# Performance work log

Measured on AMD Instinct MI355X. Metric: run time of the kernel, lower is better.

Reference implementation:

```python
import jax, jax.numpy as jnp
import numpy as np

B, S, D_IN, D_SRC, D_OUT = 128, 2048, 1024, 1024, 1024
W = 64                      # window_size
WL = 2 * W + 1              # window_length
STD_SQ = (W / 2.0) ** 2
EPS = 1e-14


def setup_inputs() -> dict:
    key = jax.random.key(0)
    ks = jax.random.split(key, 8)
    inp = jax.random.normal(ks[0], (B, D_IN), dtype=jnp.float32)
    source_hids = jax.random.normal(ks[1], (S, B, D_SRC), dtype=jnp.float32)
    # per-sample valid lengths; must satisfy L <= S - WL so the dynamic window stays in-bounds
    lengths = jax.random.randint(ks[2], (B,), 1024, S - WL + 1)
    encoder_padding_mask = jnp.arange(S)[:, None] >= lengths[None, :]  # [S, B], True = pad
    d_half = (D_IN + 1) // 2
    u = lambda k, shape, a: jax.random.uniform(k, shape, jnp.float32, -a, a)
    Wi = u(ks[3], (D_SRC, D_IN), 0.1)             # input_proj (no bias)
    Wo = u(ks[4], (D_OUT, D_IN + D_SRC), 0.1)     # output_proj (no bias)
    b1_bound = 1.0 / np.sqrt(D_IN)
    W1 = u(ks[5], (d_half, D_IN), b1_bound); b1 = u(ks[5], (d_half,), b1_bound)
    b2_bound = 1.0 / np.sqrt(d_half)
    W2 = u(ks[6], (1, d_half), b2_bound); b2 = u(ks[6], (1,), b2_bound)
    return {"input": inp, "source_hids": source_hids,
            "encoder_padding_mask": encoder_padding_mask,
            "Wi": Wi, "Wo": Wo, "W1": W1, "b1": b1, "W2": W2, "b2": b2}


def reference(input, source_hids, encoder_padding_mask, Wi, Wo, W1, b1, W2, b2):
    lengths = jnp.sum(~encoder_padding_mask, axis=0).astype(jnp.float32)  # [B]
    x = input @ Wi.T                                                      # [B, D_SRC]
    # predicted window center p = W + L * sigmoid(fc2(tanh(fc1(x))))
    p_sig = jax.nn.sigmoid(jnp.tanh(x @ W1.T + b1) @ W2.T + b2)[:, 0]     # [B]
    p = W + lengths * p_sig                                               # [B]
    window_start = jnp.round(p - W).astype(jnp.int32)                     # [B]
    positions = window_start[:, None].astype(jnp.float32) + jnp.arange(WL, dtype=jnp.float32)  # [B, WL]
    # per-sample dynamic window gather from [B, S, D]
    src_bt = jnp.transpose(source_hids, (1, 0, 2))
    selection = jax.vmap(
        lambda s, st: jax.lax.dynamic_slice(s, (st, 0), (WL, s.shape[1]))
    )(src_bt, window_start)                                               # [B, WL, D_SRC]
    gaussian = jnp.exp(-(positions - p[:, None]) ** 2 / (2.0 * STD_SQ))   # [B, WL]
    score = jnp.einsum('bd,bwd->bw', x, selection)                        # [B, WL]
    # valid absolute positions are [W, L + W); outside -> epsilon (matches torch loop)
    valid = (positions >= W) & (positions < lengths[:, None] + W)
    score = jnp.where(valid, score, EPS)
    a = jax.nn.softmax(score, axis=1) * gaussian                          # [B, WL]
    c = jnp.einsum('bw,bwd->bd', a, selection)                            # [B, D_SRC]
    out = jnp.tanh(jnp.concatenate((c, input), axis=1) @ Wo.T)            # [B, D_OUT]
    return out, a, window_start, window_start + WL
```

## Files before the change

### kernel.cpp

```cpp
#include <hip/hip_runtime.h>
#include <math.h>

#define BB   128
#define SS   2048
#define DIN  1024
#define DSRC 1024
#define DOUT 1024
#define WW   64
#define WLEN 129
#define HH   512
#define WCH  17
#define GW   136

#define OFF_WSI   0
#define OFF_P     512
#define OFF_LEN   1024
#define OFF_GTAB  4096
#define OFF_XP    73728
#define OFF_X32   4268032
#define OFF_Z1P   4792320
#define OFF_C32   6889472
#define OFF_CPART 7413760
#define OFF_MPART 11608064
#define OFF_LPART 11612160
#define OFF_SPART 11616256
#define OFF_OP    11685888
#define WS_NEED   15880192

#define DO_A    (BB*DOUT)
#define DO_WS   (DO_A + BB*WLEN)
#define DO_WE   (DO_WS + BB)

template<int NTOT, int KRANGE, bool F64OUT>
__device__ __forceinline__ void gemm16(const int gblk, const int t,
    const float* __restrict__ A, const int lda,
    const float* __restrict__ Wt, const int ldw,
    void* __restrict__ outp, float* __restrict__ alds )
{
    constexpr int NJB = NTOT / 16;
    const int jb = gblk % NJB;
    const int ks = gblk / NJB;
    const int lane = t & 63;
    const int wvid = __builtin_amdgcn_readfirstlane(t >> 6);
    const int j0 = jb * 16 + wvid * 2;
    const int k0 = ks * KRANGE;

    double dac[2][2];
    dac[0][0] = 0.0; dac[0][1] = 0.0; dac[1][0] = 0.0; dac[1][1] = 0.0;

    const float* wbase = Wt + (size_t)j0 * ldw;

    for (int kc = 0; kc < KRANGE; kc += 64) {
        const int kg = k0 + kc;
        __syncthreads();
        #pragma unroll
        for (int q = 0; q < 4; ++q) {
            const int f4 = t + 512 * q;
            const int bb = f4 >> 4, c4 = f4 & 15;
            const float4 v = *reinterpret_cast<const float4*>(A + (size_t)bb * lda + kg + c4 * 4);
            alds[(c4*4+0)*130 + bb] = v.x;
            alds[(c4*4+1)*130 + bb] = v.y;
            alds[(c4*4+2)*130 + bb] = v.z;
            alds[(c4*4+3)*130 + bb] = v.w;
        }
        __syncthreads();
        const float* wr = wbase + kg;
        #pragma unroll
        for (int kk16 = 0; kk16 < 64; kk16 += 16) {
            float fa[2][2];
            fa[0][0] = 0.f; fa[0][1] = 0.f; fa[1][0] = 0.f; fa[1][1] = 0.f;
            #pragma unroll
            for (int kk = 0; kk < 16; ++kk) {
                const int k = kk16 + kk;
                const float2 av = *reinterpret_cast<const float2*>(&alds[k*130 + 2*lane]);
                #pragma unroll
                for (int jj = 0; jj < 2; ++jj) {
                    const float wvv = wr[jj*ldw + k];
                    fa[jj][0] = fmaf(wvv, av.x, fa[jj][0]);
                    fa[jj][1] = fmaf(wvv, av.y, fa[jj][1]);
                }
            }
            #pragma unroll
            for (int jj = 0; jj < 2; ++jj) {
                dac[jj][0] += (double)fa[jj][0];
                dac[jj][1] += (double)fa[jj][1];
            }
        }
    }
    #pragma unroll
    for (int i = 0; i < 2; ++i) {
        const int b = 2*lane + i;
        const size_t base = ((size_t)ks * BB + b) * NTOT + j0;
        if constexpr (F64OUT) {
            double* o = (double*)outp;
            o[base + 0] = dac[0][i];
            o[base + 1] = dac[1][i];
        } else {
            float* o = (float*)outp;
            o[base + 0] = (float)dac[0][i];
            o[base + 1] = (float)dac[1][i];
        }
    }
}

__global__ __launch_bounds__(512)
void k_combo(const float* __restrict__ input, const float* __restrict__ Wi,
             const float* __restrict__ Wo, const unsigned char* __restrict__ mask,
             double* __restrict__ xp, float* __restrict__ op4, int* __restrict__ lengths)
{
    __shared__ __align__(16) float alds[64*130];
    const int blk = blockIdx.x, t = threadIdx.x;
    if (blk < 256) {
        gemm16<1024, 256, true>(blk, t, input, DIN, Wi, DIN, xp, alds);
    } else if (blk < 512) {
        gemm16<1024, 256, false>(blk - 256, t, input, DIN, Wo + 1024, DIN + DSRC, op4, alds);
    } else {
        const int b = blk - 512;
        const bool is_u8 = (mask[(size_t)SS*BB - 1] != 0);
        int cnt = 0;
        if (is_u8) {
            #pragma unroll
            for (int q = 0; q < 4; ++q)
                cnt += (mask[(size_t)(t + 512*q)*BB + b] != 0) ? 1 : 0;
        } else {
            const int* m32 = (const int*)mask;
            #pragma unroll
            for (int q = 0; q < 4; ++q)
                cnt += (m32[(size_t)(t + 512*q)*BB + b] != 0) ? 1 : 0;
        }
        int* red = (int*)alds;
        red[t] = cnt;
        __syncthreads();
        for (int st = 256; st >= 1; st >>= 1) {
            if (t < st) red[t] += red[t + st];
            __syncthreads();
        }
        if (t == 0) lengths[b] = SS - red[0];
    }
}

__global__ __launch_bounds__(512)
void k_xred(const double* __restrict__ xp, float* __restrict__ x32)
{
    const int i = blockIdx.x * 512 + threadIdx.x;
    double s = 0.0;
    #pragma unroll
    for (int ks = 0; ks < 4; ++ks) s += xp[(size_t)ks * (BB*DSRC) + i];
    x32[i] = (float)s;
}

__global__ __launch_bounds__(512)
void k_fc1(const float* __restrict__ x32, const float* __restrict__ W1, double* __restrict__ z1p)
{
    __shared__ __align__(16) float alds[64*130];
    gemm16<512, 256, true>(blockIdx.x, threadIdx.x, x32, DSRC, W1, DIN, z1p, alds);
}

__global__ __launch_bounds__(64)
void k_fc2(const double* __restrict__ z1p, const float* __restrict__ b1,
           const float* __restrict__ W2f, const float* __restrict__ b2,
           const int* __restrict__ lengths, int* __restrict__ wsi,
           float* __restrict__ pbuf, float* __restrict__ gtab, float* __restrict__ dout)
{
    const int b = blockIdx.x, lane = threadIdx.x;
    double part = 0.0;
    #pragma unroll
    for (int q = 0; q < 8; ++q) {
        const int h = lane + 64*q;
        double z = 0.0;
        #pragma unroll
        for (int ks = 0; ks < 4; ++ks) z += z1p[((size_t)ks*BB + b)*HH + h];
        z += (double)b1[h];
        part += tanh(z) * (double)W2f[h];
    }
    #pragma unroll
    for (int off = 32; off >= 1; off >>= 1) part += __shfl_xor(part, off);
    const double z2  = part + (double)b2[0];
    const double sig = 1.0 / (1.0 + exp(-z2));
    const double wsf = (double)lengths[b] * sig;
    int W0 = (int)rint(wsf);
    if (W0 < 0) W0 = 0;
    if (W0 > SS - WLEN) W0 = SS - WLEN;
    const float pf = (float)(wsf + 64.0);
    if (lane == 0) {
        wsi[b]  = W0;
        pbuf[b] = pf;
        dout[DO_WS + b] = (float)W0;
        dout[DO_WE + b] = (float)(W0 + WLEN);
    }
    #pragma unroll
    for (int q = 0; q < 3; ++q) {
        const int w = lane + 64*q;
        if (w < GW) {
            float g = 0.f;
            if (w < WLEN) {
                const float d = (float)(W0 + w) - pf;
                g = expf(d*d * (-1.0f/2048.0f));
            }
            gtab[b*GW + w] = g;
        }
    }
}

__global__ __launch_bounds__(256)
void k_score(const float* __restrict__ x32, const float* __restrict__ src,
             const int* __restrict__ wsi, const float* __restrict__ pbuf,
             const int* __restrict__ lengths, const float* __restrict__ gtab,
             float* __restrict__ cpart, float* __restrict__ mpart,
             float* __restrict__ lpart, float* __restrict__ spart)
{
    const int wc = blockIdx.x, b = blockIdx.y;
    const int t = threadIdx.x, lane = t & 63, wv = t >> 6;
    const int   w0 = wsi[b];
    const int   L  = lengths[b];

    const float4 x4 = *reinterpret_cast<const float4*>(x32 + b*DSRC + 4*t);

    float4 sel[WCH];
    #pragma unroll
    for (int i = 0; i < WCH; ++i) {
        const int w = wc*WCH + i;
        if (w < WLEN) {
            const size_t off = ((size_t)(w0 + w) * BB + b) * DSRC + 4*t;
            sel[i] = *reinterpret_cast<const float4*>(src + off);
        } else sel[i] = make_float4(0.f, 0.f, 0.f, 0.f);
    }

    float w_[32];
    #pragma unroll
    for (int i = 0; i < WCH; ++i)
        w_[i] = fmaf(x4.x, sel[i].x, fmaf(x4.y, sel[i].y, fmaf(x4.z, sel[i].z, x4.w * sel[i].w)));
    #pragma unroll
    for (int i = WCH; i < 32; ++i) w_[i] = 0.f;

    #pragma unroll
    for (int k = 0; k < 5; ++k) {
        const int dist = 1 << k;
        const bool hi = (lane >> k) & 1;
        const int n2 = 32 >> (k + 1);
        #pragma unroll
        for (int i = 0; i < n2; ++i) {
            const float keep = hi ? w_[2*i+1] : w_[2*i];
            const float send = hi ? w_[2*i]   : w_[2*i+1];
            w_[i] = keep + __shfl_xor(send, dist);
        }
    }
    const float tot = w_[0] + __shfl_xor(w_[0], 32);

    __shared__ float red[WCH][4];
    __shared__ float s_sh[WCH];
    if (lane < WCH) red[lane][wv] = tot;
    __syncthreads();
    if (t < WCH) {
        const int w = wc*WCH + t;
        float s;
        if (w < WLEN) {
            const float sum = red[t][0] + red[t][1] + red[t][2] + red[t][3];
            const int pos = w0 + w;
            s = (pos >= WW && pos < L + WW) ? sum : 1e-14f;
        } else s = -INFINITY;
        s_sh[t] = s;
    }
    __syncthreads();

    float sv[WCH];
    #pragma unroll
    for (int i = 0; i < WCH; ++i) sv[i] = s_sh[i];
    float m_loc = -INFINITY;
    #pragma unroll
    for (int i = 0; i < WCH; ++i) m_loc = fmaxf(m_loc, sv[i]);
    float l_loc = 0.f;
    float4 c = make_float4(0.f, 0.f, 0.f, 0.f);
    #pragma unroll
    for (int i = 0; i < WCH; ++i) {
        const float e = expf(sv[i] - m_loc);
        l_loc += e;
        const float g = gtab[b*GW + wc*WCH + i];
        const float wt = e * g;
        c.x = fmaf(wt, sel[i].x, c.x);
        c.y = fmaf(wt, sel[i].y, c.y);
        c.z = fmaf(wt, sel[i].z, c.z);
        c.w = fmaf(wt, sel[i].w, c.w);
    }
    *reinterpret_cast<float4*>(cpart + ((size_t)(b*8 + wc))*DSRC + 4*t) = c;
    if (t == 0) { mpart[b*8 + wc] = m_loc; lpart[b*8 + wc] = l_loc; }
    if (t < WCH) spart[(b*8 + wc)*WCH + t] = s_sh[t];
}

__global__ __launch_bounds__(256)
void k_merge(const float* __restrict__ cpart, const float* __restrict__ mpart,
             const float* __restrict__ lpart, const float* __restrict__ spart,
             const float* __restrict__ gtab, float* __restrict__ c32,
             float* __restrict__ dout)
{
    const int b = blockIdx.x, t = threadIdx.x;
    __shared__ float mv[8], lv[8];
    if (t < 8) { mv[t] = mpart[b*8 + t]; lv[t] = lpart[b*8 + t]; }
    __syncthreads();
    float m = -INFINITY;
    #pragma unroll
    for (int i = 0; i < 8; ++i) m = fmaxf(m, mv[i]);
    float l = 0.f;
    float fac[8];
    #pragma unroll
    for (int i = 0; i < 8; ++i) { fac[i] = expf(mv[i] - m); l = fmaf(lv[i], fac[i], l); }
    const float inv = 1.0f / l;

    float4 c = make_float4(0.f, 0.f, 0.f, 0.f);
    #pragma unroll
    for (int i = 0; i < 8; ++i) {
        const float4 cp = *reinterpret_cast<const float4*>(cpart + ((size_t)(b*8 + i))*DSRC + 4*t);
        c.x = fmaf(cp.x, fac[i], c.x);
        c.y = fmaf(cp.y, fac[i], c.y);
        c.z = fmaf(cp.z, fac[i], c.z);
        c.w = fmaf(cp.w, fac[i], c.w);
    }
    c.x *= inv; c.y *= inv; c.z *= inv; c.w *= inv;
    *reinterpret_cast<float4*>(c32 + (size_t)b*DSRC + 4*t) = c;

    if (t < WLEN) {
        const int wc = t / WCH, i = t % WCH;
        const float s = spart[(b*8 + wc)*WCH + i];
        const float g = gtab[b*GW + t];
        dout[DO_A + b*WLEN + t] = expf(s - m) * inv * g;
    }
}

__global__ __launch_bounds__(512)
void k_gemm2c(const float* __restrict__ c32, const float* __restrict__ Wo, float* __restrict__ op)
{
    __shared__ __align__(16) float alds[64*130];
    gemm16<1024, 256, false>(blockIdx.x, threadIdx.x, c32, DSRC, Wo, DIN + DSRC, op, alds);
}

__global__ __launch_bounds__(512)
void k_outred(const float* __restrict__ op, float* __restrict__ dout)
{
    const int i = blockIdx.x * 512 + threadIdx.x;
    float s = 0.f;
    #pragma unroll
    for (int ks = 0; ks < 8; ++ks) s += op[(size_t)ks * (BB*DOUT) + i];
    dout[i] = tanhf(s);
}

extern "C" void kernel_launch(void* const* d_in, const int* in_sizes, int n_in,
                              void* d_out, int out_size, void* d_ws, size_t ws_size,
                              hipStream_t stream)
{
    const float* input = (const float*)d_in[0];
    const float* src   = (const float*)d_in[1];
    const unsigned char* mask = (const unsigned char*)d_in[2];
    const float* Wi = (const float*)d_in[3];
    const float* Wo = (const float*)d_in[4];
    const float* W1 = (const float*)d_in[5];
    const float* b1 = (const float*)d_in[6];
    const float* W2 = (const float*)d_in[7];
    const float* b2 = (const float*)d_in[8];
    float* out = (float*)d_out;

    if (ws_size < (size_t)WS_NEED) return;

    char* ws = (char*)d_ws;
    int*    wsi     = (int*)   (ws + OFF_WSI);
    float*  pbuf    = (float*) (ws + OFF_P);
    int*    lengths = (int*)   (ws + OFF_LEN);
    float*  gtab    = (float*) (ws + OFF_GTAB);
    double* xp      = (double*)(ws + OFF_XP);
    float*  x32     = (float*) (ws + OFF_X32);
    double* z1p     = (double*)(ws + OFF_Z1P);
    float*  c32     = (float*) (ws + OFF_C32);
    float*  cpart   = (float*) (ws + OFF_CPART);
    float*  mpart   = (float*) (ws + OFF_MPART);
    float*  lpart   = (float*) (ws + OFF_LPART);
    float*  spart   = (float*) (ws + OFF_SPART);
    float*  op      = (float*) (ws + OFF_OP);

    k_combo<<<640, 512, 0, stream>>>(input, Wi, Wo, mask, xp, op + 4*(size_t)BB*DOUT, lengths);
    k_xred<<<256, 512, 0, stream>>>(xp, x32);
    k_fc1<<<128, 512, 0, stream>>>(x32, W1, z1p);
    k_fc2<<<128, 64, 0, stream>>>(z1p, b1, W2, b2, lengths, wsi, pbuf, gtab, out);
    k_score<<<dim3(8,128), 256, 0, stream>>>(x32, src, wsi, pbuf, lengths, gtab,
                                             cpart, mpart, lpart, spart);
    k_merge<<<128, 256, 0, stream>>>(cpart, mpart, lpart, spart, gtab, c32, out);
    k_gemm2c<<<256, 512, 0, stream>>>(c32, Wo, op);
    k_outred<<<256, 512, 0, stream>>>(op, out);
}
```

Measured before the change: 75.55 us.

## Compute Wi and Wo-input GEMMs with full-K per block, drop x reduction kernel

Replaces the split-K gemm16 calls in the first kernel with a custom full-K loop: each wave computes one output column for all 128 batch rows, staging input tiles through LDS with register prefetch. The direct results remove the k_xred launch and its partial-sum buffers, and the output reduction now reads 4 partials plus one direct term. Grid shrinks from 640 to 384 blocks, so there is less parallelism and each block does a longer serial K loop. The x32 buffer is also reused for c32, which is safe only because nothing reads x32 after k_score runs.

```diff
diff --git a/kernel.cpp b/kernel.cpp
--- a/kernel.cpp
+++ b/kernel.cpp
@@ -16,16 +16,15 @@
 #define OFF_P     512
 #define OFF_LEN   1024
 #define OFF_GTAB  4096
-#define OFF_XP    73728
-#define OFF_X32   4268032
-#define OFF_Z1P   4792320
-#define OFF_C32   6889472
-#define OFF_CPART 7413760
-#define OFF_MPART 11608064
-#define OFF_LPART 11612160
-#define OFF_SPART 11616256
-#define OFF_OP    11685888
-#define WS_NEED   15880192
+#define OFF_X32   73728
+#define OFF_OPI   598016
+#define OFF_Z1P   1122304
+#define OFF_CPART 3219456
+#define OFF_MPART 7413760
+#define OFF_LPART 7417856
+#define OFF_SPART 7421952
+#define OFF_OP    7491584
+#define WS_NEED   9588736
 
 #define DO_A    (BB*DOUT)
 #define DO_WS   (DO_A + BB*WLEN)
@@ -106,16 +105,68 @@
 __global__ __launch_bounds__(512)
 void k_combo(const float* __restrict__ input, const float* __restrict__ Wi,
              const float* __restrict__ Wo, const unsigned char* __restrict__ mask,
-             double* __restrict__ xp, float* __restrict__ op4, int* __restrict__ lengths)
+             float* __restrict__ x32, float* __restrict__ opi, int* __restrict__ lengths)
 {
     __shared__ __align__(16) float alds[64*130];
     const int blk = blockIdx.x, t = threadIdx.x;
+    const int lane = t & 63;
+    const int wv = __builtin_amdgcn_readfirstlane(t >> 6);
+
     if (blk < 256) {
-        gemm16<1024, 256, true>(blk, t, input, DIN, Wi, DIN, xp, alds);
-    } else if (blk < 512) {
-        gemm16<1024, 256, false>(blk - 256, t, input, DIN, Wo + 1024, DIN + DSRC, op4, alds);
+        const bool isX = (blk < 128);
+        const int j = (isX ? blk : blk - 128) * 8 + wv;
+        const float* wr0 = isX ? (Wi + (size_t)j * DIN)
+                               : (Wo + (size_t)j * (DIN + DSRC) + 1024);
+        double dac0 = 0.0, dac1 = 0.0;
+
+        float4 pf[4];
+        #pragma unroll
+        for (int q = 0; q < 4; ++q) {
+            const int f4 = t + 512*q;
+            const int bb = f4 >> 4, c4 = f4 & 15;
+            pf[q] = *reinterpret_cast<const float4*>(input + (size_t)bb*DIN + c4*4);
+        }
+        for (int c = 0; c < 16; ++c) {
+            __syncthreads();
+            #pragma unroll
+            for (int q = 0; q < 4; ++q) {
+                const int f4 = t + 512*q;
+                const int bb = f4 >> 4, c4 = f4 & 15;
+                alds[(c4*4+0)*130 + bb] = pf[q].x;
+                alds[(c4*4+1)*130 + bb] = pf[q].y;
+                alds[(c4*4+2)*130 + bb] = pf[q].z;
+                alds[(c4*4+3)*130 + bb] = pf[q].w;
+            }
+            __syncthreads();
+            if (c + 1 < 16) {
+                #pragma unroll
+                for (int q = 0; q < 4; ++q) {
+                    const int f4 = t + 512*q;
+                    const int bb = f4 >> 4, c4 = f4 & 15;
+                    pf[q] = *reinterpret_cast<const float4*>(input + (size_t)bb*DIN + (c+1)*64 + c4*4);
+                }
+            }
+            const float* wr = wr0 + c*64;
+            #pragma unroll
+            for (int kk16 = 0; kk16 < 64; kk16 += 16) {
+                float fa0 = 0.f, fa1 = 0.f;
+                #pragma unroll
+                for (int kk = 0; kk < 16; ++kk) {
+                    const int k = kk16 + kk;
+                    const float2 av = *reinterpret_cast<const float2*>(&alds[k*130 + 2*lane]);
+                    const float wvv = wr[k];
+                    fa0 = fmaf(wvv, av.x, fa0);
+                    fa1 = fmaf(wvv, av.y, fa1);
+                }
+                dac0 += (double)fa0;
+                dac1 += (double)fa1;
+            }
+        }
+        float* dst = isX ? x32 : opi;
+        dst[(size_t)(2*lane    )*1024 + j] = (float)dac0;
+        dst[(size_t)(2*lane + 1)*1024 + j] = (float)dac1;
     } else {
-        const int b = blk - 512;
+        const int b = blk - 256;
         const bool is_u8 = (mask[(size_t)SS*BB - 1] != 0);
         int cnt = 0;
         if (is_u8) {
@@ -137,16 +188,6 @@
         }
         if (t == 0) lengths[b] = SS - red[0];
     }
-}
-
-__global__ __launch_bounds__(512)
-void k_xred(const double* __restrict__ xp, float* __restrict__ x32)
-{
-    const int i = blockIdx.x * 512 + threadIdx.x;
-    double s = 0.0;
-    #pragma unroll
-    for (int ks = 0; ks < 4; ++ks) s += xp[(size_t)ks * (BB*DSRC) + i];
-    x32[i] = (float)s;
 }
 
 __global__ __launch_bounds__(512)
@@ -334,12 +375,14 @@
 }
 
 __global__ __launch_bounds__(512)
-void k_outred(const float* __restrict__ op, float* __restrict__ dout)
+void k_outred(const float* __restrict__ op, const float* __restrict__ opi,
+              float* __restrict__ dout)
 {
     const int i = blockIdx.x * 512 + threadIdx.x;
     float s = 0.f;
     #pragma unroll
-    for (int ks = 0; ks < 8; ++ks) s += op[(size_t)ks * (BB*DOUT) + i];
+    for (int ks = 0; ks < 4; ++ks) s += op[(size_t)ks * (BB*DOUT) + i];
+    s += opi[i];
     dout[i] = tanhf(s);
 }
 
@@ -365,23 +408,22 @@
     float*  pbuf    = (float*) (ws + OFF_P);
     int*    lengths = (int*)   (ws + OFF_LEN);
     float*  gtab    = (float*) (ws + OFF_GTAB);
-    double* xp      = (double*)(ws + OFF_XP);
     float*  x32     = (float*) (ws + OFF_X32);
+    float*  opi     = (float*) (ws + OFF_OPI);
     double* z1p     = (double*)(ws + OFF_Z1P);
-    float*  c32     = (float*) (ws + OFF_C32);
     float*  cpart   = (float*) (ws + OFF_CPART);
     float*  mpart   = (float*) (ws + OFF_MPART);
     float*  lpart   = (float*) (ws + OFF_LPART);
     float*  spart   = (float*) (ws + OFF_SPART);
     float*  op      = (float*) (ws + OFF_OP);
-
-    k_combo<<<640, 512, 0, stream>>>(input, Wi, Wo, mask, xp, op + 4*(size_t)BB*DOUT, lengths);
-    k_xred<<<256, 512, 0, stream>>>(xp, x32);
+    float*  c32     = x32;
+
+    k_combo<<<384, 512, 0, stream>>>(input, Wi, Wo, mask, x32, opi, lengths);
     k_fc1<<<128, 512, 0, stream>>>(x32, W1, z1p);
     k_fc2<<<128, 64, 0, stream>>>(z1p, b1, W2, b2, lengths, wsi, pbuf, gtab, out);
     k_score<<<dim3(8,128), 256, 0, stream>>>(x32, src, wsi, pbuf, lengths, gtab,
                                              cpart, mpart, lpart, spart);
     k_merge<<<128, 256, 0, stream>>>(cpart, mpart, lpart, spart, gtab, c32, out);
     k_gemm2c<<<256, 512, 0, stream>>>(c32, Wo, op);
-    k_outred<<<256, 512, 0, stream>>>(op, out);
-}
+    k_outred<<<256, 512, 0, stream>>>(op, opi, out);
+}
```

Measured after the change: 95.82 us. 26.8% more time.
